# Kernel optimization log

Hardware: AMD Instinct MI355X
Metric: run time of the kernel (lower is better)

The kernel has to match this reference:

```python
import jax, jax.numpy as jnp
import numpy as np

B = 8192          # number of bags/users
L = 50            # items per bag (uniform)
NNZ = B * L
VOCAB = 100000
D = 64            # embedding_dim
ATT = 64          # att_dim
K = 4             # acc_user_num


def setup_inputs() -> dict:
    key = jax.random.key(0)
    k1, k2, k3, k4, k5 = jax.random.split(key, 5)
    # flat CSR indices, sorted within each row (module assumes coalesced order)
    idx = jax.random.randint(k1, (B, L), 0, VOCAB, dtype=jnp.int64)
    input_ = jnp.sort(idx, axis=1).reshape(NNZ)
    offsets = (jnp.arange(B, dtype=jnp.int64) * L)
    emb_weight = jax.random.normal(k2, (VOCAB, D), dtype=jnp.float32) * 0.05
    proj_w = jax.random.normal(k3, (ATT, D), dtype=jnp.float32) * (1.0 / np.sqrt(D))
    proj_b = jax.random.normal(k4, (ATT,), dtype=jnp.float32) * 0.01
    att_h = jax.random.truncated_normal(k5, -2.0, 2.0, (ATT, K), dtype=jnp.float32) * 0.01
    return {"input_": input_, "offsets": offsets, "emb_weight": emb_weight,
            "proj_w": proj_w, "proj_b": proj_b, "att_h": att_h}


def reference(input_, offsets, emb_weight, proj_w, proj_b, att_h):
    nnz = input_.shape[0]
    nseg = offsets.shape[0]
    # segment id for each flat element (offsets are sorted row starts)
    seg = jnp.searchsorted(offsets, jnp.arange(nnz), side="right") - 1  # [nnz]
    att_emb = emb_weight[input_]                                        # [nnz, D]
    att = jnp.tanh(att_emb @ proj_w.T + proj_b) @ att_h                 # [nnz, K]
    # ragged per-segment softmax over each attention column
    m = jax.ops.segment_max(att, seg, num_segments=nseg)                # [B, K]
    e = jnp.exp(att - m[seg])
    s = jax.ops.segment_sum(e, seg, num_segments=nseg)                  # [B, K]
    smax = e / s[seg]                                                   # [nnz, K]
    # weighted segment-sum pooling -> [B, K, D]
    weighted = smax[:, :, None] * att_emb[:, None, :]                   # [nnz, K, D]
    result = jax.ops.segment_sum(weighted, seg, num_segments=nseg)
    return result
```

## Files before the change

### kernel.cpp

```cpp
#include <hip/hip_runtime.h>
#include <hip/hip_bf16.h>

typedef __attribute__((ext_vector_type(4))) float  f32x4;
typedef __attribute__((ext_vector_type(4))) short  s16x4;
typedef __attribute__((ext_vector_type(8))) short  s16x8;

#define SH 72

__device__ inline short f2bf(float x) {
    return __builtin_bit_cast(short, __float2bfloat16(x));
}
__device__ inline float bf2f(short s) {
    return __builtin_bit_cast(float, ((int)(unsigned short)s) << 16);
}
__device__ inline s16x8 pack8(f32x4 a, f32x4 b) {
    s16x8 r;
    r[0] = f2bf(a[0]); r[1] = f2bf(a[1]); r[2] = f2bf(a[2]); r[3] = f2bf(a[3]);
    r[4] = f2bf(b[0]); r[5] = f2bf(b[1]); r[6] = f2bf(b[2]); r[7] = f2bf(b[3]);
    return r;
}

__global__ __launch_bounds__(256) void conv_kernel(
    const float* __restrict__ emb, short* __restrict__ emb_bf, int n8)
{
    int t = blockIdx.x * 256 + threadIdx.x;
    int stride = gridDim.x * 256;
    for (int i = t; i < n8; i += stride) {
        f32x4 a = *(const f32x4*)(emb + (size_t)i * 8);
        f32x4 b = *(const f32x4*)(emb + (size_t)i * 8 + 4);
        *(s16x8*)(emb_bf + (size_t)i * 8) = pack8(a, b);
    }
}

__global__ __launch_bounds__(256, 4) void pooled_attn_kernel(
    const int*   __restrict__ input_,
    const int*   __restrict__ offsets,
    const short* __restrict__ emb_bf,
    const float* __restrict__ pw,
    const float* __restrict__ pb,
    const float* __restrict__ ah,
    float*       __restrict__ out,
    int B, int nnz)
{
    __shared__ __align__(16) short s_pw [64 * SH];
    __shared__ __align__(16) short s_ahp[2 * 64 * 8];
    __shared__ __align__(16) float s_bias[64];
    __shared__ __align__(16) short s_h_all[4][16 * SH];
    __shared__ __align__(16) float s_w_all[4][64 * 4];

    const int tid  = threadIdx.x;
    const int lane = tid & 63;
    const int wv   = tid >> 6;
    const int col  = lane & 15;
    const int quad = lane >> 4;
    short* sh = s_h_all[wv];
    float* sw = s_w_all[wv];

    {
        int r = tid >> 2, seg = tid & 3;
        const float* rp = pw + r * 64 + seg * 16;
        f32x4 a0 = *(const f32x4*)(rp);
        f32x4 a1 = *(const f32x4*)(rp + 4);
        f32x4 a2 = *(const f32x4*)(rp + 8);
        f32x4 a3 = *(const f32x4*)(rp + 12);
        *(s16x8*)(s_pw + r * SH + seg * 16)     = pack8(a0, a1);
        *(s16x8*)(s_pw + r * SH + seg * 16 + 8) = pack8(a2, a3);
    }
    if (tid < 128) {
        int c = tid >> 6, l = tid & 63;
        int q = l >> 4, cc = l & 15;
        s16x8 v;
        #pragma unroll
        for (int j = 0; j < 8; ++j) {
            int a = c * 32 + q * 8 + j;
            v[j] = (cc < 4) ? f2bf(ah[a * 4 + cc]) : (short)0;
        }
        *(s16x8*)(s_ahp + (c * 64 + l) * 8) = v;
    }
    if (tid < 64) s_bias[tid] = pb[tid];
    __syncthreads();

    const s16x8 ahA0 = *(const s16x8*)(s_ahp + lane * 8);
    const s16x8 ahA1 = *(const s16x8*)(s_ahp + (64 + lane) * 8);
    s16x8 pwA[4][2];
    #pragma unroll
    for (int mt = 0; mt < 4; ++mt) {
        pwA[mt][0] = *(const s16x8*)(s_pw + (mt * 16 + col) * SH + quad * 8);
        pwA[mt][1] = *(const s16x8*)(s_pw + (mt * 16 + col) * SH + 32 + quad * 8);
    }

    const int bag = blockIdx.x * 4 + wv;
    if (bag >= B) return;
    const int start = offsets[bag];
    const int end   = (bag + 1 < B) ? offsets[bag + 1] : nnz;
    int n = end - start;
    if (n > 64) n = 64;
    if (n < 1) {
        float* op = out + (size_t)bag * 256 + lane;
        op[0] = 0.f; op[64] = 0.f; op[128] = 0.f; op[192] = 0.f;
        return;
    }
    const int idx_l = input_[start + (lane < n ? lane : n - 1)];

    f32x4 attv[4];
    #pragma unroll
    for (int nt = 0; nt < 4; ++nt) {
        int row = __shfl(idx_l, nt * 16 + col);
        const short* rp = emb_bf + (size_t)(unsigned)row * 64 + quad * 8;
        s16x8 eB0 = *(const s16x8*)(rp);
        s16x8 eB1 = *(const s16x8*)(rp + 32);

        #pragma unroll
        for (int mt = 0; mt < 4; ++mt) {
            f32x4 acc = *(const f32x4*)(s_bias + mt * 16 + quad * 4);
            acc = __builtin_amdgcn_mfma_f32_16x16x32_bf16(pwA[mt][0], eB0, acc, 0, 0, 0);
            acc = __builtin_amdgcn_mfma_f32_16x16x32_bf16(pwA[mt][1], eB1, acc, 0, 0, 0);
            s16x4 hp;
            #pragma unroll
            for (int r = 0; r < 4; ++r) {
                float z = acc[r];
                float t2 = z * z;
                float h = z * (1.f + t2 * (-0.33333334f +
                               t2 * (0.13333333f + t2 * (-0.05396825f))));
                hp[r] = f2bf(h);
            }
            *(s16x4*)(sh + col * SH + mt * 16 + quad * 4) = hp;
        }
        f32x4 a2 = {0.f, 0.f, 0.f, 0.f};
        s16x8 b20 = *(const s16x8*)(sh + col * SH + quad * 8);
        s16x8 b21 = *(const s16x8*)(sh + col * SH + 32 + quad * 8);
        a2 = __builtin_amdgcn_mfma_f32_16x16x32_bf16(ahA0, b20, a2, 0, 0, 0);
        a2 = __builtin_amdgcn_mfma_f32_16x16x32_bf16(ahA1, b21, a2, 0, 0, 0);
        attv[nt] = a2;
    }

    f32x4 ssum = {0.f, 0.f, 0.f, 0.f};
    #pragma unroll
    for (int nt = 0; nt < 4; ++nt) {
        const bool pad = (nt * 16 + col >= n);
        #pragma unroll
        for (int k = 0; k < 4; ++k) {
            float e = __expf(attv[nt][k]);
            e = pad ? 0.f : e;
            attv[nt][k] = e;
            ssum[k] += e;
        }
    }
    if (quad == 0) {
        #pragma unroll
        for (int t = 0; t < 4; ++t)
            *(f32x4*)(sw + (t * 16 + col) * 4) = attv[t];
    }

    float eb0[16], eb1[16];
    #pragma unroll
    for (int c = 0; c < 16; ++c) {
        int row = __builtin_amdgcn_readlane(idx_l, c);
        eb0[c] = bf2f(emb_bf[(size_t)(unsigned)row * 64 + lane]);
    }
    #pragma unroll
    for (int c = 0; c < 16; ++c) {
        int row = __builtin_amdgcn_readlane(idx_l, 16 + c);
        eb1[c] = bf2f(emb_bf[(size_t)(unsigned)row * 64 + lane]);
    }

    #pragma unroll
    for (int m = 1; m <= 8; m <<= 1)
        #pragma unroll
        for (int k = 0; k < 4; ++k)
            ssum[k] += __shfl_xor(ssum[k], m, 64);
    f32x4 rs;
    #pragma unroll
    for (int k = 0; k < 4; ++k)
        rs[k] = __builtin_amdgcn_rcpf(ssum[k]);

    f32x4 po = {0.f, 0.f, 0.f, 0.f};
    #pragma unroll
    for (int t = 0; t < 4; ++t) {
        float* ebc = (t & 1) ? eb1 : eb0;
        #pragma unroll
        for (int c = 0; c < 16; ++c) {
            f32x4 w = *(const f32x4*)(sw + (t * 16 + c) * 4);
            float ev = ebc[c];
            po[0] = fmaf(w[0], ev, po[0]);
            po[1] = fmaf(w[1], ev, po[1]);
            po[2] = fmaf(w[2], ev, po[2]);
            po[3] = fmaf(w[3], ev, po[3]);
        }
        if (t < 2) {
            #pragma unroll
            for (int c = 0; c < 16; ++c) {
                int row = __builtin_amdgcn_readlane(idx_l, (t + 2) * 16 + c);
                ebc[c] = bf2f(emb_bf[(size_t)(unsigned)row * 64 + lane]);
            }
        }
    }
    float* op = out + (size_t)bag * 256 + lane;
    op[0]   = po[0] * rs[0];
    op[64]  = po[1] * rs[1];
    op[128] = po[2] * rs[2];
    op[192] = po[3] * rs[3];
}

extern "C" void kernel_launch(void* const* d_in, const int* in_sizes, int n_in,
                              void* d_out, int out_size, void* d_ws, size_t ws_size,
                              hipStream_t stream) {
    const int*   input_  = (const int*)d_in[0];
    const int*   offsets = (const int*)d_in[1];
    const float* emb     = (const float*)d_in[2];
    const float* pw      = (const float*)d_in[3];
    const float* pb      = (const float*)d_in[4];
    const float* ah      = (const float*)d_in[5];
    float* out = (float*)d_out;
    const int nnz   = in_sizes[0];
    const int B     = in_sizes[1];
    const int vocab_elems = in_sizes[2];

    short* emb_bf = (short*)d_ws;

    conv_kernel<<<1024, 256, 0, stream>>>(emb, emb_bf, vocab_elems / 8);
    pooled_attn_kernel<<<(B + 3) / 4, 256, 0, stream>>>(input_, offsets, emb_bf,
                                                        pw, pb, ah, out, B, nnz);
}
```

Baseline: 108.1 us.

## Compute weighted pooling with MFMA reusing gathered embeddings from registers

The separate second pass, which re-gathered each embedding row from global memory as scalar bf16 loads and accumulated with FMAs, is replaced. The gathered MFMA B fragments are now staged into swizzled LDS, reusing the shared-weight LDS region. Softmax weights are written as a bf16 matrix and pooling runs as 16x16x32 MFMAs fused into the projection loop. This removes the duplicate global gather and the scalar FMA loop, at the cost of bf16 rounding of the softmax weights and extra LDS traffic and synchronisation.

```diff
diff --git a/kernel.cpp b/kernel.cpp
--- a/kernel.cpp
+++ b/kernel.cpp
@@ -9,9 +9,6 @@
 
 __device__ inline short f2bf(float x) {
     return __builtin_bit_cast(short, __float2bfloat16(x));
-}
-__device__ inline float bf2f(short s) {
-    return __builtin_bit_cast(float, ((int)(unsigned short)s) << 16);
 }
 __device__ inline s16x8 pack8(f32x4 a, f32x4 b) {
     s16x8 r;
@@ -42,19 +39,22 @@
     float*       __restrict__ out,
     int B, int nnz)
 {
-    __shared__ __align__(16) short s_pw [64 * SH];
-    __shared__ __align__(16) short s_ahp[2 * 64 * 8];
+    __shared__ __align__(16) char  s_ovl[16384];
     __shared__ __align__(16) float s_bias[64];
     __shared__ __align__(16) short s_h_all[4][16 * SH];
-    __shared__ __align__(16) float s_w_all[4][64 * 4];
+    __shared__ __align__(16) short s_amat[4][1024];
 
     const int tid  = threadIdx.x;
     const int lane = tid & 63;
     const int wv   = tid >> 6;
     const int col  = lane & 15;
     const int quad = lane >> 4;
-    short* sh = s_h_all[wv];
-    float* sw = s_w_all[wv];
+
+    short* s_pw  = (short*)s_ovl;
+    short* s_ahp = (short*)(s_ovl + 9216);
+    short* sh    = s_h_all[wv];
+    short* am    = s_amat[wv];
+    short* poolw = (short*)(s_ovl + wv * 4096);
 
     {
         int r = tid >> 2, seg = tid & 3;
@@ -88,6 +88,7 @@
         pwA[mt][0] = *(const s16x8*)(s_pw + (mt * 16 + col) * SH + quad * 8);
         pwA[mt][1] = *(const s16x8*)(s_pw + (mt * 16 + col) * SH + 32 + quad * 8);
     }
+    __syncthreads();
 
     const int bag = blockIdx.x * 4 + wv;
     if (bag >= B) return;
@@ -95,26 +96,48 @@
     const int end   = (bag + 1 < B) ? offsets[bag + 1] : nnz;
     int n = end - start;
     if (n > 64) n = 64;
+    float* op = out + (size_t)bag * 256 + lane;
     if (n < 1) {
-        float* op = out + (size_t)bag * 256 + lane;
         op[0] = 0.f; op[64] = 0.f; op[128] = 0.f; op[192] = 0.f;
         return;
     }
     const int idx_l = input_[start + (lane < n ? lane : n - 1)];
 
-    f32x4 attv[4];
+    {
+        s16x8 z = {0, 0, 0, 0, 0, 0, 0, 0};
+        *(s16x8*)(am + lane * 16)     = z;
+        *(s16x8*)(am + lane * 16 + 8) = z;
+    }
+
+    s16x8 gB0[4], gB1[4];
     #pragma unroll
     for (int nt = 0; nt < 4; ++nt) {
         int row = __shfl(idx_l, nt * 16 + col);
         const short* rp = emb_bf + (size_t)(unsigned)row * 64 + quad * 8;
-        s16x8 eB0 = *(const s16x8*)(rp);
-        s16x8 eB1 = *(const s16x8*)(rp + 32);
+        gB0[nt] = *(const s16x8*)(rp);
+        gB1[nt] = *(const s16x8*)(rp + 32);
+    }
+
+    f32x4 p0 = {0,0,0,0}, p1 = {0,0,0,0}, p2 = {0,0,0,0}, p3 = {0,0,0,0};
+    f32x4 ssum = {0, 0, 0, 0};
+
+    #pragma unroll
+    for (int nt = 0; nt < 4; ++nt) {
+        {
+            int i  = ((nt & 1) << 4) + col;
+            int wb = ((((i >> 3) ^ quad) & 3) << 3) + (i & 7);
+            #pragma unroll
+            for (int j = 0; j < 8; ++j) {
+                poolw[(quad * 8 + j) * 32 + wb]        = gB0[nt][j];
+                poolw[(quad * 8 + j) * 32 + 1024 + wb] = gB1[nt][j];
+            }
+        }
 
         #pragma unroll
         for (int mt = 0; mt < 4; ++mt) {
             f32x4 acc = *(const f32x4*)(s_bias + mt * 16 + quad * 4);
-            acc = __builtin_amdgcn_mfma_f32_16x16x32_bf16(pwA[mt][0], eB0, acc, 0, 0, 0);
-            acc = __builtin_amdgcn_mfma_f32_16x16x32_bf16(pwA[mt][1], eB1, acc, 0, 0, 0);
+            acc = __builtin_amdgcn_mfma_f32_16x16x32_bf16(pwA[mt][0], gB0[nt], acc, 0, 0, 0);
+            acc = __builtin_amdgcn_mfma_f32_16x16x32_bf16(pwA[mt][1], gB1[nt], acc, 0, 0, 0);
             s16x4 hp;
             #pragma unroll
             for (int r = 0; r < 4; ++r) {
@@ -131,41 +154,41 @@
         s16x8 b21 = *(const s16x8*)(sh + col * SH + 32 + quad * 8);
         a2 = __builtin_amdgcn_mfma_f32_16x16x32_bf16(ahA0, b20, a2, 0, 0, 0);
         a2 = __builtin_amdgcn_mfma_f32_16x16x32_bf16(ahA1, b21, a2, 0, 0, 0);
-        attv[nt] = a2;
-    }
-
-    f32x4 ssum = {0.f, 0.f, 0.f, 0.f};
-    #pragma unroll
-    for (int nt = 0; nt < 4; ++nt) {
+
         const bool pad = (nt * 16 + col >= n);
+        f32x4 ev;
         #pragma unroll
         for (int k = 0; k < 4; ++k) {
-            float e = __expf(attv[nt][k]);
+            float e = __expf(a2[k]);
             e = pad ? 0.f : e;
-            attv[nt][k] = e;
-            ssum[k] += e;
-        }
-    }
-    if (quad == 0) {
-        #pragma unroll
-        for (int t = 0; t < 4; ++t)
-            *(f32x4*)(sw + (t * 16 + col) * 4) = attv[t];
-    }
-
-    float eb0[16], eb1[16];
-    #pragma unroll
-    for (int c = 0; c < 16; ++c) {
-        int row = __builtin_amdgcn_readlane(idx_l, c);
-        eb0[c] = bf2f(emb_bf[(size_t)(unsigned)row * 64 + lane]);
-    }
-    #pragma unroll
-    for (int c = 0; c < 16; ++c) {
-        int row = __builtin_amdgcn_readlane(idx_l, 16 + c);
-        eb1[c] = bf2f(emb_bf[(size_t)(unsigned)row * 64 + lane]);
-    }
-
-    #pragma unroll
-    for (int m = 1; m <= 8; m <<= 1)
+            ev[k] = e;
+            ssum[k] += (quad == 0) ? e : 0.f;
+        }
+        if (quad == 0) {
+            int item = nt * 16 + col;
+            #pragma unroll
+            for (int r = 0; r < 4; ++r)
+                am[(r * 64 + item) ^ (r << 3)] = f2bf(ev[r]);
+        }
+
+        if ((nt & 1) == 1) {
+            const int s  = nt >> 1;
+            const int c3 = col >> 3;
+            int sa = (col * 64 + (s << 5) + (quad << 3)) ^ ((col & 7) << 3);
+            s16x8 af = *(const s16x8*)(am + sa);
+            s16x8 b0 = *(const s16x8*)(poolw + (0 * 16 + col) * 32 + (((quad ^ (0 + c3)) & 3) << 3));
+            s16x8 b1 = *(const s16x8*)(poolw + (1 * 16 + col) * 32 + (((quad ^ (2 + c3)) & 3) << 3));
+            s16x8 b2 = *(const s16x8*)(poolw + (2 * 16 + col) * 32 + (((quad ^ (4 + c3)) & 3) << 3));
+            s16x8 b3 = *(const s16x8*)(poolw + (3 * 16 + col) * 32 + (((quad ^ (6 + c3)) & 3) << 3));
+            p0 = __builtin_amdgcn_mfma_f32_16x16x32_bf16(af, b0, p0, 0, 0, 0);
+            p1 = __builtin_amdgcn_mfma_f32_16x16x32_bf16(af, b1, p1, 0, 0, 0);
+            p2 = __builtin_amdgcn_mfma_f32_16x16x32_bf16(af, b2, p2, 0, 0, 0);
+            p3 = __builtin_amdgcn_mfma_f32_16x16x32_bf16(af, b3, p3, 0, 0, 0);
+        }
+    }
+
+    #pragma unroll
+    for (int m = 1; m <= 32; m <<= 1)
         #pragma unroll
         for (int k = 0; k < 4; ++k)
             ssum[k] += __shfl_xor(ssum[k], m, 64);
@@ -174,28 +197,16 @@
     for (int k = 0; k < 4; ++k)
         rs[k] = __builtin_amdgcn_rcpf(ssum[k]);
 
-    f32x4 po = {0.f, 0.f, 0.f, 0.f};
-    #pragma unroll
-    for (int t = 0; t < 4; ++t) {
-        float* ebc = (t & 1) ? eb1 : eb0;
-        #pragma unroll
-        for (int c = 0; c < 16; ++c) {
-            f32x4 w = *(const f32x4*)(sw + (t * 16 + c) * 4);
-            float ev = ebc[c];
-            po[0] = fmaf(w[0], ev, po[0]);
-            po[1] = fmaf(w[1], ev, po[1]);
-            po[2] = fmaf(w[2], ev, po[2]);
-            po[3] = fmaf(w[3], ev, po[3]);
-        }
-        if (t < 2) {
-            #pragma unroll
-            for (int c = 0; c < 16; ++c) {
-                int row = __builtin_amdgcn_readlane(idx_l, (t + 2) * 16 + c);
-                ebc[c] = bf2f(emb_bf[(size_t)(unsigned)row * 64 + lane]);
-            }
-        }
-    }
-    float* op = out + (size_t)bag * 256 + lane;
+    asm volatile("" ::: "memory");
+    float* om = (float*)am;
+    if (quad == 0) {
+        { int d =      col; int sl = (d & 56) | ((d + (d >> 3)) & 7); *(f32x4*)(om + sl * 4) = p0; }
+        { int d = 16 + col; int sl = (d & 56) | ((d + (d >> 3)) & 7); *(f32x4*)(om + sl * 4) = p1; }
+        { int d = 32 + col; int sl = (d & 56) | ((d + (d >> 3)) & 7); *(f32x4*)(om + sl * 4) = p2; }
+        { int d = 48 + col; int sl = (d & 56) | ((d + (d >> 3)) & 7); *(f32x4*)(om + sl * 4) = p3; }
+    }
+    int sl = (lane & 56) | ((lane + (lane >> 3)) & 7);
+    f32x4 po = *(const f32x4*)(om + sl * 4);
     op[0]   = po[0] * rs[0];
     op[64]  = po[1] * rs[1];
     op[128] = po[2] * rs[2];
```

Measured after the change: 105.6 us. 1.02x faster.
